# Kernel optimization log

Measured on AMD Instinct MI355X. Metric: run time of the kernel, lower is better.

## Reference

```python
import jax, jax.numpy as jnp
import numpy as np

NUM_SPEAKERS = 8192  # static stand-in for labels.max()+1
MARGIN = 0.2
EPS = 1e-12  # torch F.normalize default eps


def _l2_normalize(x, axis=1):
    norm = jnp.linalg.norm(x, axis=axis, keepdims=True)
    return x / jnp.maximum(norm, EPS)


def setup_inputs() -> dict:
    key = jax.random.key(0)
    k1, k2 = jax.random.split(key)
    embeddings = jax.random.normal(k1, (8192, 256), dtype=jnp.float32)
    labels = jax.random.randint(k2, (8192,), 0, NUM_SPEAKERS, dtype=jnp.int32)
    return {"embeddings": embeddings, "labels": labels}


def reference(embeddings, labels):
    # Normalize embeddings: [B, D]
    e = _l2_normalize(embeddings, axis=1)
    B = e.shape[0]

    # Scatter-mean prototypes per speaker (replaces the python for-loop):
    sums = jax.ops.segment_sum(e, labels, num_segments=NUM_SPEAKERS)          # [S, D]
    counts = jax.ops.segment_sum(jnp.ones((B,), e.dtype), labels,
                                 num_segments=NUM_SPEAKERS)                    # [S]
    protos = sums / jnp.maximum(counts, 1.0)[:, None]  # zero rows stay zero like torch skip
    protos = _l2_normalize(protos, axis=1)

    # Cosine similarity: [B, S]
    cos_sim = jnp.matmul(e, protos.T)

    # Positive similarity at target column: [B]
    positive_sim = jnp.take_along_axis(cos_sim, labels[:, None].astype(jnp.int32), axis=1)[:, 0]

    # Faithful to original: subtract margin on the diagonal (requires B == S)
    cos_sim_m = cos_sim - MARGIN * jnp.eye(NUM_SPEAKERS, dtype=cos_sim.dtype)
    negative_sim = jnp.max(cos_sim_m, axis=1)

    loss = jnp.mean(jax.nn.relu(negative_sim - positive_sim + MARGIN))
    return loss
```

## Files before the change

### kernel.cpp

```cpp
#include <hip/hip_runtime.h>
#include <hip/hip_bf16.h>

typedef __attribute__((ext_vector_type(8))) short short8;
typedef __attribute__((ext_vector_type(4))) float f32x4;

#define B_ROWS 8192
#define DIM 256
#define CS 8
#define NT 16
#define NSLICE (CS * 2)
#define MARGIN_F 0.2f
#define BUCKET_CAP 32

__device__ __forceinline__ unsigned short f2bf(float x) {
  unsigned int u = __float_as_uint(x);
  unsigned int r = (u + 0x7fffu + ((u >> 16) & 1u)) >> 16;
  return (unsigned short)r;
}
__device__ __forceinline__ float bf2f(unsigned short h) {
  return __uint_as_float(((unsigned int)h) << 16);
}

__device__ __forceinline__ void gload_lds16(const void* g, void* l) {
  __builtin_amdgcn_global_load_lds(
      (const __attribute__((address_space(1))) unsigned int*)g,
      (__attribute__((address_space(3))) unsigned int*)l, 16, 0, 0);
}

__global__ __launch_bounds__(256) void k_norm_index(
    const float* __restrict__ emb, const int* __restrict__ labels,
    unsigned short* __restrict__ ebf, int* __restrict__ cursor,
    int* __restrict__ bucket) {
  int wid = threadIdx.x >> 6, lane = threadIdx.x & 63;
  int row = blockIdx.x * 4 + wid;
  const float4 v = *reinterpret_cast<const float4*>(emb + row * DIM + lane * 4);
  float ss = v.x * v.x + v.y * v.y + v.z * v.z + v.w * v.w;
#pragma unroll
  for (int off = 32; off > 0; off >>= 1) ss += __shfl_xor(ss, off);
  float scale = 1.0f / fmaxf(sqrtf(ss), 1e-12f);
  ushort4 ob;
  ob.x = f2bf(v.x * scale); ob.y = f2bf(v.y * scale);
  ob.z = f2bf(v.z * scale); ob.w = f2bf(v.w * scale);
  *reinterpret_cast<ushort4*>(ebf + row * DIM + lane * 4) = ob;
  if (lane == 0) {
    int lab = labels[row];
    int slot = atomicAdd(cursor + lab, 1);
    if (slot < BUCKET_CAP) bucket[lab * BUCKET_CAP + slot] = row;
  }
}

__global__ __launch_bounds__(256) void k_protos_gather(
    const unsigned short* __restrict__ ebf, const int* __restrict__ cursor,
    const int* __restrict__ bucket, unsigned short* __restrict__ pfrag,
    float* __restrict__ pos) {
  int wid = threadIdx.x >> 6, lane = threadIdx.x & 63;
  int p = blockIdx.x * 4 + wid;
  int c = cursor[p];
  if (c > BUCKET_CAP) c = BUCKET_CAP;
  float a0 = 0.f, a1 = 0.f, a2 = 0.f, a3 = 0.f;
  for (int k = 0; k < c; ++k) {
    int row = bucket[p * BUCKET_CAP + k];
    ushort4 ev = *reinterpret_cast<const ushort4*>(ebf + row * DIM + lane * 4);
    a0 += bf2f(ev.x); a1 += bf2f(ev.y); a2 += bf2f(ev.z); a3 += bf2f(ev.w);
  }
  float ss = a0 * a0 + a1 * a1 + a2 * a2 + a3 * a3;
#pragma unroll
  for (int off = 32; off > 0; off >>= 1) ss += __shfl_xor(ss, off);
  float scale = 1.0f / fmaxf(sqrtf(ss), 1e-12f);
  ushort4 ob;
  ob.x = f2bf(a0 * scale); ob.y = f2bf(a1 * scale);
  ob.z = f2bf(a2 * scale); ob.w = f2bf(a3 * scale);
  int addr = (p >> 6) * 16384 + ((((p >> 4) & 3) * 8 + (lane >> 3)) * 512) +
             ((((lane >> 1) & 3) * 16 + (p & 15)) * 8) + ((lane & 1) * 4);
  *reinterpret_cast<ushort4*>(pfrag + addr) = ob;
  float p0 = bf2f(ob.x), p1 = bf2f(ob.y), p2 = bf2f(ob.z), p3 = bf2f(ob.w);
  for (int k = 0; k < c; ++k) {
    int row = bucket[p * BUCKET_CAP + k];
    ushort4 ev = *reinterpret_cast<const ushort4*>(ebf + row * DIM + lane * 4);
    float d = bf2f(ev.x) * p0 + bf2f(ev.y) * p1 + bf2f(ev.z) * p2 +
              bf2f(ev.w) * p3;
#pragma unroll
    for (int off = 32; off > 0; off >>= 1) d += __shfl_xor(d, off);
    if (lane == 0) pos[row] = d;
  }
}

__global__ __attribute__((amdgpu_flat_work_group_size(256, 256)))
__attribute__((amdgpu_waves_per_eu(2, 2))) void k_gemm_negmax(
    const unsigned short* __restrict__ E, const unsigned short* __restrict__ PF,
    float* __restrict__ negp) {
  __shared__ unsigned short smbuf[2][32 * 512];
  const int tid = threadIdx.x;
  const int lane = tid & 63, wid = tid >> 6;
  const int l16 = lane & 15, lk = lane >> 4;
  const int wr = (wid >> 1) * 64;
  const int wch = wid & 1;
  const int rowBase = blockIdx.x * 128;
  const int colBase0 = blockIdx.y * 1024;
  const int tile0 = blockIdx.y * NT;

  auto stageB = [&](int buf, int tile) {
#pragma unroll
    for (int it = 0; it < 8; ++it) {
      int c = it * 4 + wid;
      gload_lds16(PF + tile * 16384 + c * 512 + lane * 8,
                  &smbuf[buf][c * 512 + lane * 8]);
    }
  };

  stageB(0, tile0);

  short8 areg[4][8];
#pragma unroll
  for (int m = 0; m < 4; ++m)
#pragma unroll
    for (int ks = 0; ks < 8; ++ks)
      areg[m][ks] = *reinterpret_cast<const short8*>(
          E + (rowBase + wr + m * 16 + l16) * DIM + ks * 32 + lk * 8);

  float rmax[4][4];
#pragma unroll
  for (int m = 0; m < 4; ++m)
#pragma unroll
    for (int r = 0; r < 4; ++r) rmax[m][r] = -3.0e38f;

  __syncthreads();

  for (int ct = 0; ct < NT; ++ct) {
    if (ct + 1 < NT) stageB((ct + 1) & 1, tile0 + ct + 1);

    const unsigned short* bs = smbuf[ct & 1];
    f32x4 acc[4][2] = {};
#pragma unroll
    for (int ks = 0; ks < 8; ++ks) {
      short8 b[2];
#pragma unroll
      for (int n = 0; n < 2; ++n)
        b[n] = *reinterpret_cast<const short8*>(
            bs + ((wch * 2 + n) * 8 + ks) * 512 + lane * 8);
#pragma unroll
      for (int m = 0; m < 4; ++m)
#pragma unroll
        for (int n = 0; n < 2; ++n)
          acc[m][n] = __builtin_amdgcn_mfma_f32_16x16x32_bf16(
              areg[m][ks], b[n], acc[m][n], 0, 0, 0);
    }

    const int colT = colBase0 + ct * 64 + wch * 32;
#pragma unroll
    for (int m = 0; m < 4; ++m) {
      int growb = rowBase + wr + m * 16 + lk * 4;
#pragma unroll
      for (int n = 0; n < 2; ++n) {
        int gcol = colT + n * 16 + l16;
#pragma unroll
        for (int r = 0; r < 4; ++r) {
          float v = acc[m][n][r];
          if (growb + r == gcol) v -= MARGIN_F;
          rmax[m][r] = fmaxf(rmax[m][r], v);
        }
      }
    }

    __syncthreads();
  }

  const int slice = blockIdx.y * 2 + wch;
#pragma unroll
  for (int m = 0; m < 4; ++m) {
#pragma unroll
    for (int r = 0; r < 4; ++r) {
      float v = rmax[m][r];
      v = fmaxf(v, __shfl_xor(v, 1));
      v = fmaxf(v, __shfl_xor(v, 2));
      v = fmaxf(v, __shfl_xor(v, 4));
      v = fmaxf(v, __shfl_xor(v, 8));
      if (l16 == 0) {
        int grow = rowBase + wr + m * 16 + lk * 4 + r;
        negp[slice * B_ROWS + grow] = v;
      }
    }
  }
}

__global__ __launch_bounds__(256) void k_loss(
    const float* __restrict__ negp, const float* __restrict__ pos,
    float* __restrict__ out) {
  int tid = threadIdx.x;
  float s = 0.f;
  for (int i = tid; i < B_ROWS; i += 256) {
    float n = negp[i];
#pragma unroll
    for (int sl = 1; sl < NSLICE; ++sl) n = fmaxf(n, negp[sl * B_ROWS + i]);
    s += fmaxf(n - pos[i] + MARGIN_F, 0.f);
  }
#pragma unroll
  for (int off = 32; off > 0; off >>= 1) s += __shfl_xor(s, off);
  __shared__ float red[4];
  if ((tid & 63) == 0) red[tid >> 6] = s;
  __syncthreads();
  if (tid == 0) out[0] = (red[0] + red[1] + red[2] + red[3]) * (1.0f / B_ROWS);
}

extern "C" void kernel_launch(void* const* d_in, const int* in_sizes, int n_in,
                              void* d_out, int out_size, void* d_ws, size_t ws_size,
                              hipStream_t stream) {
  const float* emb = (const float*)d_in[0];
  const int* labels = (const int*)d_in[1];

  char* ws = (char*)d_ws;
  int* cursor = (int*)ws;
  int* bucket = (int*)(ws + 32 * 1024);
  unsigned short* ebf =
      (unsigned short*)(ws + 32 * 1024 + 1024 * 1024);
  unsigned short* pfrag =
      (unsigned short*)(ws + 32 * 1024 + 5 * 1024 * 1024);
  float* pos = (float*)(ws + 32 * 1024 + 9 * 1024 * 1024);
  float* negp = (float*)(ws + 64 * 1024 + 9 * 1024 * 1024);

  hipMemsetAsync(cursor, 0, 32 * 1024, stream);
  k_norm_index<<<B_ROWS / 4, 256, 0, stream>>>(emb, labels, ebf, cursor, bucket);
  k_protos_gather<<<B_ROWS / 4, 256, 0, stream>>>(ebf, cursor, bucket, pfrag, pos);
  k_gemm_negmax<<<dim3(64, CS), 256, 0, stream>>>(ebf, pfrag, negp);
  k_loss<<<1, 256, 0, stream>>>(negp, pos, (float*)d_out);
}
```

Baseline: 121.2 us.

## Deepen GEMM B-tile pipeline to four LDS buffers with 512-thread blocks

The negmax GEMM moves to 512-thread blocks covering 256 rows, so each staged prototype tile is shared by twice as many waves. The tile ring grows to four buffers in 128KB of dynamic LDS, prefetching three tiles ahead, and explicit vmcnt waits replace the full __syncthreads after each tile. The final loss reduction is spread over 32 blocks that accumulate with atomicAdd, and the output is zeroed in the first kernel. In exchange, the GEMM grid shrinks to 256 blocks and the large LDS allocation limits occupancy, and the vmcnt counts are hand-tuned and fragile.

```diff
diff --git a/kernel.cpp b/kernel.cpp
--- a/kernel.cpp
+++ b/kernel.cpp
@@ -12,6 +12,8 @@
 #define MARGIN_F 0.2f
 #define BUCKET_CAP 32
 
+#define WAITV(n) asm volatile("s_waitcnt vmcnt(" #n ")" ::: "memory")
+
 __device__ __forceinline__ unsigned short f2bf(float x) {
   unsigned int u = __float_as_uint(x);
   unsigned int r = (u + 0x7fffu + ((u >> 16) & 1u)) >> 16;
@@ -30,7 +32,8 @@
 __global__ __launch_bounds__(256) void k_norm_index(
     const float* __restrict__ emb, const int* __restrict__ labels,
     unsigned short* __restrict__ ebf, int* __restrict__ cursor,
-    int* __restrict__ bucket) {
+    int* __restrict__ bucket, float* __restrict__ out) {
+  if (blockIdx.x == 0 && threadIdx.x == 0) out[0] = 0.f;
   int wid = threadIdx.x >> 6, lane = threadIdx.x & 63;
   int row = blockIdx.x * 4 + wid;
   const float4 v = *reinterpret_cast<const float4*>(emb + row * DIM + lane * 4);
@@ -85,30 +88,32 @@
   }
 }
 
-__global__ __attribute__((amdgpu_flat_work_group_size(256, 256)))
+__global__ __attribute__((amdgpu_flat_work_group_size(512, 512)))
 __attribute__((amdgpu_waves_per_eu(2, 2))) void k_gemm_negmax(
     const unsigned short* __restrict__ E, const unsigned short* __restrict__ PF,
     float* __restrict__ negp) {
-  __shared__ unsigned short smbuf[2][32 * 512];
+  extern __shared__ unsigned short smb[];
   const int tid = threadIdx.x;
   const int lane = tid & 63, wid = tid >> 6;
   const int l16 = lane & 15, lk = lane >> 4;
   const int wr = (wid >> 1) * 64;
   const int wch = wid & 1;
-  const int rowBase = blockIdx.x * 128;
+  const int rowBase = blockIdx.x * 256;
   const int colBase0 = blockIdx.y * 1024;
   const int tile0 = blockIdx.y * NT;
 
   auto stageB = [&](int buf, int tile) {
 #pragma unroll
-    for (int it = 0; it < 8; ++it) {
-      int c = it * 4 + wid;
+    for (int it = 0; it < 4; ++it) {
+      int c = it * 8 + wid;
       gload_lds16(PF + tile * 16384 + c * 512 + lane * 8,
-                  &smbuf[buf][c * 512 + lane * 8]);
+                  &smb[buf * 16384 + c * 512 + lane * 8]);
     }
   };
 
   stageB(0, tile0);
+  stageB(1, tile0 + 1);
+  stageB(2, tile0 + 2);
 
   short8 areg[4][8];
 #pragma unroll
@@ -124,12 +129,11 @@
 #pragma unroll
     for (int r = 0; r < 4; ++r) rmax[m][r] = -3.0e38f;
 
-  __syncthreads();
-
-  for (int ct = 0; ct < NT; ++ct) {
-    if (ct + 1 < NT) stageB((ct + 1) & 1, tile0 + ct + 1);
-
-    const unsigned short* bs = smbuf[ct & 1];
+  WAITV(0);
+  __builtin_amdgcn_s_barrier();
+
+  auto body = [&](int ct) {
+    const unsigned short* bs = &smb[(ct & 3) * 16384];
     f32x4 acc[4][2] = {};
 #pragma unroll
     for (int ks = 0; ks < 8; ++ks) {
@@ -145,7 +149,6 @@
           acc[m][n] = __builtin_amdgcn_mfma_f32_16x16x32_bf16(
               areg[m][ks], b[n], acc[m][n], 0, 0, 0);
     }
-
     const int colT = colBase0 + ct * 64 + wch * 32;
 #pragma unroll
     for (int m = 0; m < 4; ++m) {
@@ -161,9 +164,21 @@
         }
       }
     }
-
-    __syncthreads();
-  }
+  };
+
+  for (int ct = 0; ct < NT - 3; ++ct) {
+    body(ct);
+    stageB((ct + 3) & 3, tile0 + ct + 3);
+    WAITV(8);
+    __builtin_amdgcn_s_barrier();
+  }
+  body(13);
+  WAITV(4);
+  __builtin_amdgcn_s_barrier();
+  body(14);
+  WAITV(0);
+  __builtin_amdgcn_s_barrier();
+  body(15);
 
   const int slice = blockIdx.y * 2 + wch;
 #pragma unroll
@@ -183,23 +198,21 @@
   }
 }
 
-__global__ __launch_bounds__(256) void k_loss(
+__global__ __launch_bounds__(256) void k_loss_part(
     const float* __restrict__ negp, const float* __restrict__ pos,
     float* __restrict__ out) {
-  int tid = threadIdx.x;
-  float s = 0.f;
-  for (int i = tid; i < B_ROWS; i += 256) {
-    float n = negp[i];
-#pragma unroll
-    for (int sl = 1; sl < NSLICE; ++sl) n = fmaxf(n, negp[sl * B_ROWS + i]);
-    s += fmaxf(n - pos[i] + MARGIN_F, 0.f);
-  }
-#pragma unroll
-  for (int off = 32; off > 0; off >>= 1) s += __shfl_xor(s, off);
+  int i = blockIdx.x * 256 + threadIdx.x;
+  float n = negp[i];
+#pragma unroll
+  for (int s = 1; s < NSLICE; ++s) n = fmaxf(n, negp[s * B_ROWS + i]);
+  float t = fmaxf(n - pos[i] + MARGIN_F, 0.f);
+#pragma unroll
+  for (int off = 32; off > 0; off >>= 1) t += __shfl_xor(t, off);
   __shared__ float red[4];
-  if ((tid & 63) == 0) red[tid >> 6] = s;
+  if ((threadIdx.x & 63) == 0) red[threadIdx.x >> 6] = t;
   __syncthreads();
-  if (tid == 0) out[0] = (red[0] + red[1] + red[2] + red[3]) * (1.0f / B_ROWS);
+  if (threadIdx.x == 0)
+    atomicAdd(out, (red[0] + red[1] + red[2] + red[3]) * (1.0f / B_ROWS));
 }
 
 extern "C" void kernel_launch(void* const* d_in, const int* in_sizes, int n_in,
@@ -219,8 +232,11 @@
   float* negp = (float*)(ws + 64 * 1024 + 9 * 1024 * 1024);
 
   hipMemsetAsync(cursor, 0, 32 * 1024, stream);
-  k_norm_index<<<B_ROWS / 4, 256, 0, stream>>>(emb, labels, ebf, cursor, bucket);
+  k_norm_index<<<B_ROWS / 4, 256, 0, stream>>>(emb, labels, ebf, cursor, bucket,
+                                               (float*)d_out);
   k_protos_gather<<<B_ROWS / 4, 256, 0, stream>>>(ebf, cursor, bucket, pfrag, pos);
-  k_gemm_negmax<<<dim3(64, CS), 256, 0, stream>>>(ebf, pfrag, negp);
-  k_loss<<<1, 256, 0, stream>>>(negp, pos, (float*)d_out);
-}
+  hipFuncSetAttribute((const void*)k_gemm_negmax,
+                      hipFuncAttributeMaxDynamicSharedMemorySize, 131072);
+  k_gemm_negmax<<<dim3(32, CS), 512, 131072, stream>>>(ebf, pfrag, negp);
+  k_loss_part<<<32, 256, 0, stream>>>(negp, pos, (float*)d_out);
+}
```

New measurement: 105.9 us. 12.7% less time.
